# Kernel tuning notes

Measured on AMD Instinct MI355X. Metric: run time of the kernel, lower is better.

Reference implementation:

```python
import jax, jax.numpy as jnp
import numpy as np

T, H, I = 4096, 4096, 11008  # tokens, hidden_size, intermediate_size
QMAX = 127.0


def setup_inputs() -> dict:
    key = jax.random.key(0)
    k0, k1, k2, k3, k4 = jax.random.split(key, 5)
    x = jax.random.normal(k0, (T, H), dtype=jnp.float32)
    # int8 weights stored as float32 integer values in [-127, 127]
    wq_gate_up = jnp.round(jnp.clip(jax.random.normal(k1, (2 * I, H), dtype=jnp.float32) * 30.0, -QMAX, QMAX))
    s_gate_up = jax.random.uniform(k2, (2 * I,), dtype=jnp.float32, minval=5e-4, maxval=2e-3)
    wq_down = jnp.round(jnp.clip(jax.random.normal(k3, (H, I), dtype=jnp.float32) * 30.0, -QMAX, QMAX))
    s_down = jax.random.uniform(k4, (H,), dtype=jnp.float32, minval=5e-4, maxval=2e-3)
    return {"x": x, "wq_gate_up": wq_gate_up, "s_gate_up": s_gate_up,
            "wq_down": wq_down, "s_down": s_down}


def reference(x, wq_gate_up, s_gate_up, wq_down, s_down):
    # --- quantize activations (per-tensor dynamic int8) ---
    x_scale = jnp.max(jnp.abs(x)) / QMAX
    qx = jnp.clip(jnp.round(x / x_scale), -QMAX, QMAX)  # integer-valued f32 (simulated int8)

    # --- gate_up_proj: int8 GEMM (int32 accumulate simulated in f32) ---
    acc = qx @ wq_gate_up.T                             # [T, 2I]
    gate_up = acc * (x_scale * s_gate_up)               # dequant: per-tensor act * per-channel weight scale

    # --- DequantSiluAndMulQuant: silu(gate) * up, then dynamic requant ---
    gate, up = jnp.split(gate_up, 2, axis=-1)           # [T, I] each
    h = jax.nn.silu(gate) * up
    h_scale = jnp.max(jnp.abs(h)) / QMAX
    qh = jnp.clip(jnp.round(h / h_scale), -QMAX, QMAX)

    # --- down_proj: int8 GEMM + dequant ---
    out = (qh @ wq_down.T) * (h_scale * s_down)         # [T, H]
    return out, h_scale
```

## Files before the change

kernel.cpp:

```cpp
#include <hip/hip_runtime.h>

#define T_DIM 4096
#define K1    4096
#define I_DIM 11008
#define QMAXF 127.0f

typedef int v4i __attribute__((ext_vector_type(4)));


__device__ __forceinline__ void gload16(const void* g, void* l) {
  __builtin_amdgcn_global_load_lds((__attribute__((address_space(1))) unsigned int*)(g),
                                   (__attribute__((address_space(3))) unsigned int*)(l),
                                   16, 0, 0);
}

__device__ __forceinline__ int packq(float a, float b, float c, float d) {
  return ((int)a & 255) | (((int)b & 255) << 8) | (((int)c & 255) << 16) | (((int)d & 255) << 24);
}


__global__ void absmax_x_kernel(const float4* __restrict__ x4, unsigned* __restrict__ maxbits, int n4) {
  int tid = blockIdx.x * blockDim.x + threadIdx.x;
  int stride = gridDim.x * blockDim.x;
  float m = 0.f;
  for (int i = tid; i < n4; i += stride) {
    float4 v = x4[i];
    m = fmaxf(m, fmaxf(fmaxf(fabsf(v.x), fabsf(v.y)), fmaxf(fabsf(v.z), fabsf(v.w))));
  }
  #pragma unroll
  for (int off = 32; off; off >>= 1) m = fmaxf(m, __shfl_xor(m, off));
  if ((threadIdx.x & 63) == 0) atomicMax(maxbits, __float_as_uint(m));
}


__global__ void quant_x_kernel(const float4* __restrict__ x4, v4i* __restrict__ q4,
                               const unsigned* __restrict__ scal) {
  const float sx = __uint_as_float(scal[0]) * (1.0f / QMAXF);
  const long i = (long)blockIdx.x * blockDim.x + threadIdx.x;
  v4i o;
  #pragma unroll
  for (int j = 0; j < 4; ++j) {
    float4 v = x4[i * 4 + j];
    float a = fminf(fmaxf(rintf(v.x / sx), -QMAXF), QMAXF);
    float b = fminf(fmaxf(rintf(v.y / sx), -QMAXF), QMAXF);
    float c = fminf(fmaxf(rintf(v.z / sx), -QMAXF), QMAXF);
    float d = fminf(fmaxf(rintf(v.w / sx), -QMAXF), QMAXF);
    o[j] = packq(a, b, c, d);
  }
  q4[i] = o;
}


__global__ void conv_w_kernel(const float4* __restrict__ w4, v4i* __restrict__ q4) {
  const long i = (long)blockIdx.x * blockDim.x + threadIdx.x;
  v4i o;
  #pragma unroll
  for (int j = 0; j < 4; ++j) {
    float4 v = w4[i * 4 + j];
    o[j] = packq(rintf(v.x), rintf(v.y), rintf(v.z), rintf(v.w));
  }
  q4[i] = o;
}


__global__ __launch_bounds__(512, 2)
void gemm1_silu_kernel(const signed char* __restrict__ qx,
                       const signed char* __restrict__ w8,
                       const float* __restrict__ sgu,
                       unsigned* __restrict__ scal,
                       float* __restrict__ hbuf)
{
  __shared__ signed char As[3][16384];
  __shared__ signed char Bs[3][16384];

  const int tid  = threadIdx.x;
  const int lane = tid & 63;
  const int wid  = tid >> 6;
  const int wr   = wid >> 2;
  const int wc   = wid & 3;
  const int ln15 = lane & 15;
  const int klg  = lane >> 4;

  const int lin = blockIdx.x;
  const int sw  = (lin & 7) * 172 + (lin >> 3);
  const int brow = (sw & 15) * 256;
  const int bcol = (sw >> 4) * 128;

  const int sr = tid & 127, ss = tid >> 7;
  const signed char* gA0 = qx + (size_t)(brow + sr) * K1 + ss * 16;
  const signed char* gA1 = qx + (size_t)(brow + 128 + sr) * K1 + ss * 16;
  const signed char* gB0 = w8 + (size_t)(bcol + sr) * K1 + ss * 16;
  const signed char* gB1 = w8 + (size_t)(I_DIM + bcol + sr) * K1 + ss * 16;
  const int l0 = tid * 16, l1 = 8192 + tid * 16;

  const int abase = wr * 8192 + klg * 2048 + ln15 * 16;
  const int gbase = klg * 2048 + (wc * 32 + ln15) * 16;

  v4i zero = {0, 0, 0, 0};
  v4i accg[8][2], accu[8][2];
  #pragma unroll
  for (int m = 0; m < 8; ++m)
    #pragma unroll
    for (int n = 0; n < 2; ++n) { accg[m][n] = zero; accu[m][n] = zero; }

  auto stage01 = [&](int kt, int b) {
    gload16(gA0 + kt * 64, &As[b][l0]);
    gload16(gB0 + kt * 64, &Bs[b][l0]);
  };
  auto stage23 = [&](int kt, int b) {
    gload16(gA1 + kt * 64, &As[b][l1]);
    gload16(gB1 + kt * 64, &Bs[b][l1]);
  };

  stage01(0, 0); stage23(0, 0);
  stage01(1, 1); stage23(1, 1);

  const int nk = K1 / 64;
  int cb = 0, sb = 2;
  for (int kt = 0; kt < nk; ++kt) {
    if (kt < nk - 1) asm volatile("s_waitcnt vmcnt(4)" ::: "memory");
    else             asm volatile("s_waitcnt vmcnt(0)" ::: "memory");
    __builtin_amdgcn_s_barrier();
    asm volatile("" ::: "memory");
    const signed char* A = As[cb];
    const signed char* B = Bs[cb];

    v4i af[4], bg0, bg1, bu0, bu1;
    #pragma unroll
    for (int m = 0; m < 4; ++m) af[m] = *(const v4i*)&A[abase + m * 256];
    bg0 = *(const v4i*)&B[gbase];
    bg1 = *(const v4i*)&B[gbase + 256];
    bu0 = *(const v4i*)&B[8192 + gbase];
    bu1 = *(const v4i*)&B[8192 + gbase + 256];
    if (kt + 2 < nk) stage01(kt + 2, sb);
    __builtin_amdgcn_s_barrier();
    asm volatile("s_waitcnt lgkmcnt(0)" ::: "memory");
    __builtin_amdgcn_sched_barrier(0);
    __builtin_amdgcn_s_setprio(1);
    #pragma unroll
    for (int m = 0; m < 4; ++m) {
      accg[m][0] = __builtin_amdgcn_mfma_i32_16x16x64_i8(af[m], bg0, accg[m][0], 0, 0, 0);
      accg[m][1] = __builtin_amdgcn_mfma_i32_16x16x64_i8(af[m], bg1, accg[m][1], 0, 0, 0);
      accu[m][0] = __builtin_amdgcn_mfma_i32_16x16x64_i8(af[m], bu0, accu[m][0], 0, 0, 0);
      accu[m][1] = __builtin_amdgcn_mfma_i32_16x16x64_i8(af[m], bu1, accu[m][1], 0, 0, 0);
    }
    __builtin_amdgcn_s_setprio(0);

    v4i af2[4];
    #pragma unroll
    for (int m = 0; m < 4; ++m) af2[m] = *(const v4i*)&A[abase + 1024 + m * 256];
    if (kt + 2 < nk) stage23(kt + 2, sb);
    __builtin_amdgcn_s_barrier();
    asm volatile("s_waitcnt lgkmcnt(0)" ::: "memory");
    __builtin_amdgcn_sched_barrier(0);
    __builtin_amdgcn_s_setprio(1);
    #pragma unroll
    for (int m = 0; m < 4; ++m) {
      accg[m + 4][0] = __builtin_amdgcn_mfma_i32_16x16x64_i8(af2[m], bg0, accg[m + 4][0], 0, 0, 0);
      accg[m + 4][1] = __builtin_amdgcn_mfma_i32_16x16x64_i8(af2[m], bg1, accg[m + 4][1], 0, 0, 0);
      accu[m + 4][0] = __builtin_amdgcn_mfma_i32_16x16x64_i8(af2[m], bu0, accu[m + 4][0], 0, 0, 0);
      accu[m + 4][1] = __builtin_amdgcn_mfma_i32_16x16x64_i8(af2[m], bu1, accu[m + 4][1], 0, 0, 0);
    }
    __builtin_amdgcn_s_setprio(0);

    cb = (cb + 1 == 3) ? 0 : cb + 1;
    sb = (sb + 1 == 3) ? 0 : sb + 1;
  }

  const float xsc = __uint_as_float(scal[0]) * (1.0f / QMAXF);
  float hmax = 0.f;
  #pragma unroll
  for (int m = 0; m < 8; ++m) {
    const int row0 = brow + wr * 128 + m * 16 + klg * 4;
    #pragma unroll
    for (int n = 0; n < 2; ++n) {
      const int col = bcol + wc * 32 + n * 16 + ln15;
      const float sg = sgu[col] * xsc;
      const float su = sgu[I_DIM + col] * xsc;
      #pragma unroll
      for (int q = 0; q < 4; ++q) {
        float g = (float)accg[m][n][q] * sg;
        float u = (float)accu[m][n][q] * su;
        float hv = (g / (1.f + expf(-g))) * u;
        hmax = fmaxf(hmax, fabsf(hv));
        hbuf[(size_t)(row0 + q) * I_DIM + col] = hv;
      }
    }
  }
  #pragma unroll
  for (int off = 32; off; off >>= 1) hmax = fmaxf(hmax, __shfl_xor(hmax, off));
  if (lane == 0) atomicMax(scal + 1, __float_as_uint(hmax));
}


__global__ void quant_h_kernel(const float4* __restrict__ h4, v4i* __restrict__ q4,
                               const unsigned* __restrict__ scal) {
  const float hs = __uint_as_float(scal[1]) * (1.0f / QMAXF);
  const long i = (long)blockIdx.x * blockDim.x + threadIdx.x;
  v4i o;
  #pragma unroll
  for (int j = 0; j < 4; ++j) {
    float4 v = h4[i * 4 + j];
    float a = fminf(fmaxf(rintf(v.x / hs), -QMAXF), QMAXF);
    float b = fminf(fmaxf(rintf(v.y / hs), -QMAXF), QMAXF);
    float c = fminf(fmaxf(rintf(v.z / hs), -QMAXF), QMAXF);
    float d = fminf(fmaxf(rintf(v.w / hs), -QMAXF), QMAXF);
    o[j] = packq(a, b, c, d);
  }
  q4[i] = o;
}

__global__ void hscale_out_kernel(const unsigned* __restrict__ scal, float* __restrict__ dst) {
  dst[0] = __uint_as_float(scal[1]) * (1.0f / QMAXF);
}


__global__ __launch_bounds__(512, 4)
void gemm2_kernel(const signed char* __restrict__ qh,
                  const signed char* __restrict__ w8,
                  const float* __restrict__ sdn,
                  const unsigned* __restrict__ scal,
                  float* __restrict__ out)
{
  __shared__ signed char As[3][16384];
  __shared__ signed char Bs[3][8192];

  const int tid  = threadIdx.x;
  const int lane = tid & 63;
  const int wid  = tid >> 6;
  const int wr   = wid >> 1;
  const int wc   = wid & 1;
  const int ln15 = lane & 15;
  const int klg  = lane >> 4;

  const int lin = blockIdx.x;
  const int sw  = (lin & 7) * 64 + (lin >> 3);
  const int brow = (sw & 15) * 256;
  const int bcol = (sw >> 4) * 128;

  const int sr = tid & 127, ss = tid >> 7;
  const signed char* gA0 = qh + (size_t)(brow + sr) * I_DIM + ss * 16;
  const signed char* gA1 = qh + (size_t)(brow + 128 + sr) * I_DIM + ss * 16;
  const signed char* gB  = w8 + (size_t)(bcol + sr) * I_DIM + ss * 16;
  const int l0 = tid * 16, l1 = 8192 + tid * 16;

  const int abase = (wr >> 1) * 8192 + klg * 2048 + ((wr & 1) * 64 + ln15) * 16;
  const int bbase = klg * 2048 + (wc * 64 + ln15) * 16;

  v4i zero = {0, 0, 0, 0};
  v4i acc[4][4];
  #pragma unroll
  for (int m = 0; m < 4; ++m)
    #pragma unroll
    for (int n = 0; n < 4; ++n) acc[m][n] = zero;

  auto stage = [&](int kt, int b) {
    gload16(gA0 + kt * 64, &As[b][l0]);
    gload16(gA1 + kt * 64, &As[b][l1]);
    gload16(gB  + kt * 64, &Bs[b][tid * 16]);
  };

  stage(0, 0);
  stage(1, 1);
  const int nk = I_DIM / 64;
  int cb = 0, sb = 2;
  for (int kt = 0; kt < nk; ++kt) {
    if (kt < nk - 1) asm volatile("s_waitcnt vmcnt(3)" ::: "memory");
    else             asm volatile("s_waitcnt vmcnt(0)" ::: "memory");
    __builtin_amdgcn_s_barrier();
    asm volatile("" ::: "memory");
    const signed char* A = As[cb];
    const signed char* B = Bs[cb];

    v4i af[4], bf[4];
    #pragma unroll
    for (int m = 0; m < 4; ++m) af[m] = *(const v4i*)&A[abase + m * 256];
    #pragma unroll
    for (int n = 0; n < 4; ++n) bf[n] = *(const v4i*)&B[bbase + n * 256];
    if (kt + 2 < nk) stage(kt + 2, sb);
    __builtin_amdgcn_s_barrier();
    asm volatile("s_waitcnt lgkmcnt(0)" ::: "memory");
    __builtin_amdgcn_sched_barrier(0);
    __builtin_amdgcn_s_setprio(1);
    #pragma unroll
    for (int m = 0; m < 4; ++m)
      #pragma unroll
      for (int n = 0; n < 4; ++n)
        acc[m][n] = __builtin_amdgcn_mfma_i32_16x16x64_i8(af[m], bf[n], acc[m][n], 0, 0, 0);
    __builtin_amdgcn_s_setprio(0);

    cb = (cb + 1 == 3) ? 0 : cb + 1;
    sb = (sb + 1 == 3) ? 0 : sb + 1;
  }

  const float hsc = __uint_as_float(scal[1]) * (1.0f / QMAXF);
  #pragma unroll
  for (int m = 0; m < 4; ++m) {
    const int row0 = brow + wr * 64 + m * 16 + klg * 4;
    #pragma unroll
    for (int n = 0; n < 4; ++n) {
      const int col = bcol + wc * 64 + n * 16 + ln15;
      const float s = sdn[col] * hsc;
      #pragma unroll
      for (int q = 0; q < 4; ++q)
        out[(size_t)(row0 + q) * K1 + col] = (float)acc[m][n][q] * s;
    }
  }
}


extern "C" void kernel_launch(void* const* d_in, const int* in_sizes, int n_in,
                              void* d_out, int out_size, void* d_ws, size_t ws_size,
                              hipStream_t stream) {
  (void)in_sizes; (void)n_in; (void)out_size; (void)ws_size;
  const float* x   = (const float*)d_in[0];
  const float* wgu = (const float*)d_in[1];
  const float* sgu = (const float*)d_in[2];
  const float* wdn = (const float*)d_in[3];
  const float* sdn = (const float*)d_in[4];
  float* out = (float*)d_out;
  char* ws = (char*)d_ws;

  signed char* qx  = (signed char*)(ws + 0LL);
  signed char* w8g = (signed char*)(ws + 16777216LL);
  signed char* w8d = (signed char*)(ws + 106954752LL);
  signed char* qh  = (signed char*)(ws + 152043520LL);
  float*       hb  = (float*)      (ws + 197132288LL);
  unsigned*    scal= (unsigned*)   (ws + 377487360LL);

  hipMemsetAsync(scal, 0, 256, stream);
  absmax_x_kernel<<<2048, 256, 0, stream>>>((const float4*)x, scal, T_DIM * K1 / 4);
  quant_x_kernel<<<4096, 256, 0, stream>>>((const float4*)x, (v4i*)qx, scal);
  conv_w_kernel<<<22016, 256, 0, stream>>>((const float4*)wgu, (v4i*)w8g);
  conv_w_kernel<<<11008, 256, 0, stream>>>((const float4*)wdn, (v4i*)w8d);

  gemm1_silu_kernel<<<1376, 512, 0, stream>>>(qx, w8g, sgu, scal, hb);

  quant_h_kernel<<<11008, 256, 0, stream>>>((const float4*)hb, (v4i*)qh, scal);
  hscale_out_kernel<<<1, 1, 0, stream>>>(scal, out + (size_t)T_DIM * K1);

  gemm2_kernel<<<512, 512, 0, stream>>>(qh, w8d, sdn, scal, out);
}
```

Baseline: 1.321 ms.

## Restructure both int8 GEMMs with unified 4-stage LDS pipeline and 256x256 down-proj tiles

Both GEMM kernels now share one 128KB LDS array split into four stages instead of three. The K loop is unrolled by four so buffer indices are compile-time constants, and each k-tile is split into two phases, each issuing half of the next stage's global-to-LDS loads. gemm1 interleaves gate and up weight rows in one B tile and uses a single 8x4 accumulator array. gemm2 grows from 256x128 to 256x256 tiles on 256 blocks to get more operand reuse per LDS load, at the cost of lower occupancy (one block per CU given the LDS size) and less latency hiding across blocks.

Measured after the change: 1.187 ms. 1.11x faster.

```diff
diff --git a/kernel.cpp b/kernel.cpp
--- a/kernel.cpp
+++ b/kernel.cpp
@@ -5,7 +5,7 @@
 #define I_DIM 11008
 #define QMAXF 127.0f
 
-typedef int v4i __attribute__((ext_vector_type(4)));
+typedef int v4i  __attribute__((ext_vector_type(4)));
 
 
 __device__ __forceinline__ void gload16(const void* g, void* l) {
@@ -17,6 +17,8 @@
 __device__ __forceinline__ int packq(float a, float b, float c, float d) {
   return ((int)a & 255) | (((int)b & 255) << 8) | (((int)c & 255) << 16) | (((int)d & 255) << 24);
 }
+
+#define MFMA(A, B, C) __builtin_amdgcn_mfma_i32_16x16x64_i8(A, B, C, 0, 0, 0)
 
 
 __global__ void absmax_x_kernel(const float4* __restrict__ x4, unsigned* __restrict__ maxbits, int n4) {
@@ -63,6 +65,63 @@
 }
 
 
+#define STG_A(PTR, SB) { gload16((PTR), &L[SB][lA]); gload16((PTR) + 32, &L[SB][lA + 8192]); }
+#define STG_B(PTR, SB) { gload16((PTR), &L[SB][lB]); gload16((PTR) + 32, &L[SB][lB + 8192]); }
+
+#define PH0(CB, SB, APTR, DOST)                                              \
+  {                                                                          \
+    a0 = *(const v4i*)&L[CB][aoff];                                          \
+    a1 = *(const v4i*)&L[CB][aoff + 256];                                    \
+    a2 = *(const v4i*)&L[CB][aoff + 512];                                    \
+    a3 = *(const v4i*)&L[CB][aoff + 768];                                    \
+    b0 = *(const v4i*)&L[CB][boff];                                          \
+    b1 = *(const v4i*)&L[CB][boff + 256];                                    \
+    b2 = *(const v4i*)&L[CB][boff + 512];                                    \
+    b3 = *(const v4i*)&L[CB][boff + 768];                                    \
+    if (DOST) STG_A(APTR, SB);                                               \
+    __builtin_amdgcn_s_barrier();                                            \
+    asm volatile("s_waitcnt lgkmcnt(0)" ::: "memory");                       \
+    __builtin_amdgcn_sched_barrier(0);                                       \
+    __builtin_amdgcn_s_setprio(1);                                           \
+    acc[0][0]=MFMA(a0,b0,acc[0][0]); acc[0][1]=MFMA(a0,b1,acc[0][1]);        \
+    acc[0][2]=MFMA(a0,b2,acc[0][2]); acc[0][3]=MFMA(a0,b3,acc[0][3]);        \
+    acc[1][0]=MFMA(a1,b0,acc[1][0]); acc[1][1]=MFMA(a1,b1,acc[1][1]);        \
+    acc[1][2]=MFMA(a1,b2,acc[1][2]); acc[1][3]=MFMA(a1,b3,acc[1][3]);        \
+    acc[2][0]=MFMA(a2,b0,acc[2][0]); acc[2][1]=MFMA(a2,b1,acc[2][1]);        \
+    acc[2][2]=MFMA(a2,b2,acc[2][2]); acc[2][3]=MFMA(a2,b3,acc[2][3]);        \
+    acc[3][0]=MFMA(a3,b0,acc[3][0]); acc[3][1]=MFMA(a3,b1,acc[3][1]);        \
+    acc[3][2]=MFMA(a3,b2,acc[3][2]); acc[3][3]=MFMA(a3,b3,acc[3][3]);        \
+    __builtin_amdgcn_s_setprio(0);                                           \
+    __builtin_amdgcn_s_barrier();                                            \
+    asm volatile("" ::: "memory");                                           \
+  }
+
+#define PH1(CB, SB, BPTR, DOST, VM)                                          \
+  {                                                                          \
+    a0 = *(const v4i*)&L[CB][aoff + 1024];                                   \
+    a1 = *(const v4i*)&L[CB][aoff + 1280];                                   \
+    a2 = *(const v4i*)&L[CB][aoff + 1536];                                   \
+    a3 = *(const v4i*)&L[CB][aoff + 1792];                                   \
+    if (DOST) STG_B(BPTR, SB);                                               \
+    __builtin_amdgcn_s_barrier();                                            \
+    asm volatile("s_waitcnt lgkmcnt(0)" ::: "memory");                       \
+    __builtin_amdgcn_sched_barrier(0);                                       \
+    __builtin_amdgcn_s_setprio(1);                                           \
+    acc[4][0]=MFMA(a0,b0,acc[4][0]); acc[4][1]=MFMA(a0,b1,acc[4][1]);        \
+    acc[4][2]=MFMA(a0,b2,acc[4][2]); acc[4][3]=MFMA(a0,b3,acc[4][3]);        \
+    acc[5][0]=MFMA(a1,b0,acc[5][0]); acc[5][1]=MFMA(a1,b1,acc[5][1]);        \
+    acc[5][2]=MFMA(a1,b2,acc[5][2]); acc[5][3]=MFMA(a1,b3,acc[5][3]);        \
+    acc[6][0]=MFMA(a2,b0,acc[6][0]); acc[6][1]=MFMA(a2,b1,acc[6][1]);        \
+    acc[6][2]=MFMA(a2,b2,acc[6][2]); acc[6][3]=MFMA(a2,b3,acc[6][3]);        \
+    acc[7][0]=MFMA(a3,b0,acc[7][0]); acc[7][1]=MFMA(a3,b1,acc[7][1]);        \
+    acc[7][2]=MFMA(a3,b2,acc[7][2]); acc[7][3]=MFMA(a3,b3,acc[7][3]);        \
+    __builtin_amdgcn_s_setprio(0);                                           \
+    asm volatile("s_waitcnt vmcnt(" VM ")" ::: "memory");                    \
+    __builtin_amdgcn_s_barrier();                                            \
+    asm volatile("" ::: "memory");                                           \
+  }
+
+
 __global__ __launch_bounds__(512, 2)
 void gemm1_silu_kernel(const signed char* __restrict__ qx,
                        const signed char* __restrict__ w8,
@@ -70,8 +129,7 @@
                        unsigned* __restrict__ scal,
                        float* __restrict__ hbuf)
 {
-  __shared__ signed char As[3][16384];
-  __shared__ signed char Bs[3][16384];
+  __shared__ signed char L[4][32768];
 
   const int tid  = threadIdx.x;
   const int lane = tid & 63;
@@ -79,99 +137,57 @@
   const int wr   = wid >> 2;
   const int wc   = wid & 3;
   const int ln15 = lane & 15;
-  const int klg  = lane >> 4;
+  const int kq   = lane >> 4;
 
   const int lin = blockIdx.x;
   const int sw  = (lin & 7) * 172 + (lin >> 3);
   const int brow = (sw & 15) * 256;
   const int bcol = (sw >> 4) * 128;
 
-  const int sr = tid & 127, ss = tid >> 7;
-  const signed char* gA0 = qx + (size_t)(brow + sr) * K1 + ss * 16;
-  const signed char* gA1 = qx + (size_t)(brow + 128 + sr) * K1 + ss * 16;
-  const signed char* gB0 = w8 + (size_t)(bcol + sr) * K1 + ss * 16;
-  const signed char* gB1 = w8 + (size_t)(I_DIM + bcol + sr) * K1 + ss * 16;
-  const int l0 = tid * 16, l1 = 8192 + tid * 16;
-
-  const int abase = wr * 8192 + klg * 2048 + ln15 * 16;
-  const int gbase = klg * 2048 + (wc * 32 + ln15) * 16;
-
-  v4i zero = {0, 0, 0, 0};
-  v4i accg[8][2], accu[8][2];
+  const int sro = tid & 255, skq = tid >> 8;
+  const signed char* gA = qx + (size_t)(brow + sro) * K1 + skq * 16;
+  const int grp = sro >> 6, w = sro & 63;
+  const int gcolw = bcol + grp * 32 + (w & 31);
+  const size_t srcrow = (w < 32) ? (size_t)gcolw : (size_t)(I_DIM + gcolw);
+  const signed char* gB = w8 + srcrow * K1 + skq * 16;
+  const int lA = tid * 16;
+  const int lB = 16384 + tid * 16;
+
+  const int aoff = kq * 4096 + (wr * 128 + ln15) * 16;
+  const int boff = 16384 + kq * 4096 + (wc * 64 + ln15) * 16;
+
+  v4i acc[8][4];
   #pragma unroll
   for (int m = 0; m < 8; ++m)
     #pragma unroll
-    for (int n = 0; n < 2; ++n) { accg[m][n] = zero; accu[m][n] = zero; }
-
-  auto stage01 = [&](int kt, int b) {
-    gload16(gA0 + kt * 64, &As[b][l0]);
-    gload16(gB0 + kt * 64, &Bs[b][l0]);
-  };
-  auto stage23 = [&](int kt, int b) {
-    gload16(gA1 + kt * 64, &As[b][l1]);
-    gload16(gB1 + kt * 64, &Bs[b][l1]);
-  };
-
-  stage01(0, 0); stage23(0, 0);
-  stage01(1, 1); stage23(1, 1);
-
-  const int nk = K1 / 64;
-  int cb = 0, sb = 2;
-  for (int kt = 0; kt < nk; ++kt) {
-    if (kt < nk - 1) asm volatile("s_waitcnt vmcnt(4)" ::: "memory");
-    else             asm volatile("s_waitcnt vmcnt(0)" ::: "memory");
-    __builtin_amdgcn_s_barrier();
-    asm volatile("" ::: "memory");
-    const signed char* A = As[cb];
-    const signed char* B = Bs[cb];
-
-    v4i af[4], bg0, bg1, bu0, bu1;
-    #pragma unroll
-    for (int m = 0; m < 4; ++m) af[m] = *(const v4i*)&A[abase + m * 256];
-    bg0 = *(const v4i*)&B[gbase];
-    bg1 = *(const v4i*)&B[gbase + 256];
-    bu0 = *(const v4i*)&B[8192 + gbase];
-    bu1 = *(const v4i*)&B[8192 + gbase + 256];
-    if (kt + 2 < nk) stage01(kt + 2, sb);
-    __builtin_amdgcn_s_barrier();
-    asm volatile("s_waitcnt lgkmcnt(0)" ::: "memory");
-    __builtin_amdgcn_sched_barrier(0);
-    __builtin_amdgcn_s_setprio(1);
-    #pragma unroll
-    for (int m = 0; m < 4; ++m) {
-      accg[m][0] = __builtin_amdgcn_mfma_i32_16x16x64_i8(af[m], bg0, accg[m][0], 0, 0, 0);
-      accg[m][1] = __builtin_amdgcn_mfma_i32_16x16x64_i8(af[m], bg1, accg[m][1], 0, 0, 0);
-      accu[m][0] = __builtin_amdgcn_mfma_i32_16x16x64_i8(af[m], bu0, accu[m][0], 0, 0, 0);
-      accu[m][1] = __builtin_amdgcn_mfma_i32_16x16x64_i8(af[m], bu1, accu[m][1], 0, 0, 0);
-    }
-    __builtin_amdgcn_s_setprio(0);
-
-    v4i af2[4];
-    #pragma unroll
-    for (int m = 0; m < 4; ++m) af2[m] = *(const v4i*)&A[abase + 1024 + m * 256];
-    if (kt + 2 < nk) stage23(kt + 2, sb);
-    __builtin_amdgcn_s_barrier();
-    asm volatile("s_waitcnt lgkmcnt(0)" ::: "memory");
-    __builtin_amdgcn_sched_barrier(0);
-    __builtin_amdgcn_s_setprio(1);
-    #pragma unroll
-    for (int m = 0; m < 4; ++m) {
-      accg[m + 4][0] = __builtin_amdgcn_mfma_i32_16x16x64_i8(af2[m], bg0, accg[m + 4][0], 0, 0, 0);
-      accg[m + 4][1] = __builtin_amdgcn_mfma_i32_16x16x64_i8(af2[m], bg1, accg[m + 4][1], 0, 0, 0);
-      accu[m + 4][0] = __builtin_amdgcn_mfma_i32_16x16x64_i8(af2[m], bu0, accu[m + 4][0], 0, 0, 0);
-      accu[m + 4][1] = __builtin_amdgcn_mfma_i32_16x16x64_i8(af2[m], bu1, accu[m + 4][1], 0, 0, 0);
-    }
-    __builtin_amdgcn_s_setprio(0);
-
-    cb = (cb + 1 == 3) ? 0 : cb + 1;
-    sb = (sb + 1 == 3) ? 0 : sb + 1;
-  }
+    for (int n = 0; n < 4; ++n) acc[m][n] = v4i{0, 0, 0, 0};
+  v4i a0, a1, a2, a3, b0, b1, b2, b3;
+
+  STG_A(gA, 0); STG_B(gB, 0);
+  STG_A(gA + 64, 1); STG_B(gB + 64, 1);
+  asm volatile("s_waitcnt vmcnt(4)" ::: "memory");
+  __builtin_amdgcn_s_barrier();
+  asm volatile("" ::: "memory");
+
+  const signed char* gAp = gA;
+  const signed char* gBp = gB;
+  for (int p = 0; p < 15; ++p) {
+    PH0(0, 2, gAp + 128, 1) PH1(0, 2, gBp + 128, 1, "4")
+    PH0(1, 3, gAp + 192, 1) PH1(1, 3, gBp + 192, 1, "4")
+    PH0(2, 0, gAp + 256, 1) PH1(2, 0, gBp + 256, 1, "4")
+    PH0(3, 1, gAp + 320, 1) PH1(3, 1, gBp + 320, 1, "4")
+    gAp += 256; gBp += 256;
+  }
+  PH0(0, 2, gAp + 128, 1) PH1(0, 2, gBp + 128, 1, "4")
+  PH0(1, 3, gAp + 192, 1) PH1(1, 3, gBp + 192, 1, "4")
+  PH0(2, 0, gAp,       0) PH1(2, 0, gBp,       0, "0")
+  PH0(3, 1, gAp,       0) PH1(3, 1, gBp,       0, "0")
 
   const float xsc = __uint_as_float(scal[0]) * (1.0f / QMAXF);
   float hmax = 0.f;
   #pragma unroll
   for (int m = 0; m < 8; ++m) {
-    const int row0 = brow + wr * 128 + m * 16 + klg * 4;
+    const int row0 = brow + wr * 128 + m * 16 + kq * 4;
     #pragma unroll
     for (int n = 0; n < 2; ++n) {
       const int col = bcol + wc * 32 + n * 16 + ln15;
@@ -179,8 +195,8 @@
       const float su = sgu[I_DIM + col] * xsc;
       #pragma unroll
       for (int q = 0; q < 4; ++q) {
-        float g = (float)accg[m][n][q] * sg;
-        float u = (float)accu[m][n][q] * su;
+        float g = (float)acc[m][n][q] * sg;
+        float u = (float)acc[m][n + 2][q] * su;
         float hv = (g / (1.f + expf(-g))) * u;
         hmax = fmaxf(hmax, fabsf(hv));
         hbuf[(size_t)(row0 + q) * I_DIM + col] = hv;
@@ -215,88 +231,68 @@
 }
 
 
-__global__ __launch_bounds__(512, 4)
+__global__ __launch_bounds__(512, 2)
 void gemm2_kernel(const signed char* __restrict__ qh,
                   const signed char* __restrict__ w8,
                   const float* __restrict__ sdn,
                   const unsigned* __restrict__ scal,
                   float* __restrict__ out)
 {
-  __shared__ signed char As[3][16384];
-  __shared__ signed char Bs[3][8192];
+  __shared__ signed char L[4][32768];
 
   const int tid  = threadIdx.x;
   const int lane = tid & 63;
   const int wid  = tid >> 6;
-  const int wr   = wid >> 1;
-  const int wc   = wid & 1;
+  const int wr   = wid >> 2;
+  const int wc   = wid & 3;
   const int ln15 = lane & 15;
-  const int klg  = lane >> 4;
+  const int kq   = lane >> 4;
 
   const int lin = blockIdx.x;
-  const int sw  = (lin & 7) * 64 + (lin >> 3);
+  const int sw  = (lin & 7) * 32 + (lin >> 3);
   const int brow = (sw & 15) * 256;
-  const int bcol = (sw >> 4) * 128;
-
-  const int sr = tid & 127, ss = tid >> 7;
-  const signed char* gA0 = qh + (size_t)(brow + sr) * I_DIM + ss * 16;
-  const signed char* gA1 = qh + (size_t)(brow + 128 + sr) * I_DIM + ss * 16;
-  const signed char* gB  = w8 + (size_t)(bcol + sr) * I_DIM + ss * 16;
-  const int l0 = tid * 16, l1 = 8192 + tid * 16;
-
-  const int abase = (wr >> 1) * 8192 + klg * 2048 + ((wr & 1) * 64 + ln15) * 16;
-  const int bbase = klg * 2048 + (wc * 64 + ln15) * 16;
-
-  v4i zero = {0, 0, 0, 0};
-  v4i acc[4][4];
-  #pragma unroll
-  for (int m = 0; m < 4; ++m)
+  const int bcol = (sw >> 4) * 256;
+
+  const int sro = tid & 255, skq = tid >> 8;
+  const signed char* gA = qh + (size_t)(brow + sro) * I_DIM + skq * 16;
+  const signed char* gB = w8 + (size_t)(bcol + sro) * I_DIM + skq * 16;
+  const int lA = tid * 16;
+  const int lB = 16384 + tid * 16;
+
+  const int aoff = kq * 4096 + (wr * 128 + ln15) * 16;
+  const int boff = 16384 + kq * 4096 + (wc * 64 + ln15) * 16;
+
+  v4i acc[8][4];
+  #pragma unroll
+  for (int m = 0; m < 8; ++m)
     #pragma unroll
-    for (int n = 0; n < 4; ++n) acc[m][n] = zero;
-
-  auto stage = [&](int kt, int b) {
-    gload16(gA0 + kt * 64, &As[b][l0]);
-    gload16(gA1 + kt * 64, &As[b][l1]);
-    gload16(gB  + kt * 64, &Bs[b][tid * 16]);
-  };
-
-  stage(0, 0);
-  stage(1, 1);
-  const int nk = I_DIM / 64;
-  int cb = 0, sb = 2;
-  for (int kt = 0; kt < nk; ++kt) {
-    if (kt < nk - 1) asm volatile("s_waitcnt vmcnt(3)" ::: "memory");
-    else             asm volatile("s_waitcnt vmcnt(0)" ::: "memory");
-    __builtin_amdgcn_s_barrier();
-    asm volatile("" ::: "memory");
-    const signed char* A = As[cb];
-    const signed char* B = Bs[cb];
-
-    v4i af[4], bf[4];
-    #pragma unroll
-    for (int m = 0; m < 4; ++m) af[m] = *(const v4i*)&A[abase + m * 256];
-    #pragma unroll
-    for (int n = 0; n < 4; ++n) bf[n] = *(const v4i*)&B[bbase + n * 256];
-    if (kt + 2 < nk) stage(kt + 2, sb);
-    __builtin_amdgcn_s_barrier();
-    asm volatile("s_waitcnt lgkmcnt(0)" ::: "memory");
-    __builtin_amdgcn_sched_barrier(0);
-    __builtin_amdgcn_s_setprio(1);
-    #pragma unroll
-    for (int m = 0; m < 4; ++m)
-      #pragma unroll
-      for (int n = 0; n < 4; ++n)
-        acc[m][n] = __builtin_amdgcn_mfma_i32_16x16x64_i8(af[m], bf[n], acc[m][n], 0, 0, 0);
-    __builtin_amdgcn_s_setprio(0);
-
-    cb = (cb + 1 == 3) ? 0 : cb + 1;
-    sb = (sb + 1 == 3) ? 0 : sb + 1;
-  }
+    for (int n = 0; n < 4; ++n) acc[m][n] = v4i{0, 0, 0, 0};
+  v4i a0, a1, a2, a3, b0, b1, b2, b3;
+
+  STG_A(gA, 0); STG_B(gB, 0);
+  STG_A(gA + 64, 1); STG_B(gB + 64, 1);
+  asm volatile("s_waitcnt vmcnt(4)" ::: "memory");
+  __builtin_amdgcn_s_barrier();
+  asm volatile("" ::: "memory");
+
+  const signed char* gAp = gA;
+  const signed char* gBp = gB;
+  for (int p = 0; p < 42; ++p) {
+    PH0(0, 2, gAp + 128, 1) PH1(0, 2, gBp + 128, 1, "4")
+    PH0(1, 3, gAp + 192, 1) PH1(1, 3, gBp + 192, 1, "4")
+    PH0(2, 0, gAp + 256, 1) PH1(2, 0, gBp + 256, 1, "4")
+    PH0(3, 1, gAp + 320, 1) PH1(3, 1, gBp + 320, 1, "4")
+    gAp += 256; gBp += 256;
+  }
+  PH0(0, 2, gAp + 128, 1) PH1(0, 2, gBp + 128, 1, "4")
+  PH0(1, 3, gAp + 192, 1) PH1(1, 3, gBp + 192, 1, "4")
+  PH0(2, 0, gAp,       0) PH1(2, 0, gBp,       0, "0")
+  PH0(3, 1, gAp,       0) PH1(3, 1, gBp,       0, "0")
 
   const float hsc = __uint_as_float(scal[1]) * (1.0f / QMAXF);
   #pragma unroll
-  for (int m = 0; m < 4; ++m) {
-    const int row0 = brow + wr * 64 + m * 16 + klg * 4;
+  for (int m = 0; m < 8; ++m) {
+    const int row0 = brow + wr * 128 + m * 16 + kq * 4;
     #pragma unroll
     for (int n = 0; n < 4; ++n) {
       const int col = bcol + wc * 64 + n * 16 + ln15;
@@ -339,5 +335,5 @@
   quant_h_kernel<<<11008, 256, 0, stream>>>((const float4*)hb, (v4i*)qh, scal);
   hscale_out_kernel<<<1, 1, 0, stream>>>(scal, out + (size_t)T_DIM * K1);
 
-  gemm2_kernel<<<512, 512, 0, stream>>>(qh, w8d, sdn, scal, out);
-}
+  gemm2_kernel<<<256, 512, 0, stream>>>(qh, w8d, sdn, scal, out);
+}
```
